# Kernel tuning notes

Hardware: AMD Instinct MI355X
Metric: run time of the kernel (lower is better)

Reference implementation:

```python
import jax, jax.numpy as jnp
import numpy as np
from jax import lax


def setup_inputs() -> dict:
    key = jax.random.key(0)
    # [C=512, H=256, W=256] feature map
    x = jax.random.normal(key, (512, 256, 256), dtype=jnp.float32)
    return {"x": x}


def reference(x):
    # Original torch forward mutates x in place: _bottom_pool (cummax down rows,
    # axis=1) modifies x and returns it, then _right_pool (cummax across cols,
    # axis=2) runs on the SAME already-bottom-pooled tensor. Thus `bottom` and
    # `right` alias and out = 2 * cummax_w(cummax_h(x)).
    y = lax.cummax(lax.cummax(x, axis=1), axis=2)
    return y + y
```

## Files before the change

kernel.cpp:

```cpp
#include <hip/hip_runtime.h>
#include <math.h>

#define CC 512
#define HH 256
#define WW 256
#define RB 32
#define NTILES (HH / RB)
#define NT 256
#define RPW (RB / 4)

typedef float f32x4 __attribute__((ext_vector_type(4)));

#define BAR()    asm volatile("s_barrier" ::: "memory")
#define WAITV(N) asm volatile("s_waitcnt vmcnt(" #N ")" ::: "memory")
#define WAITL()  asm volatile("s_waitcnt lgkmcnt(0)" ::: "memory")

template<int CTRL, int ROW_MASK>
__device__ __forceinline__ float dpp_ninf(float v) {
    union { float f; int i; } o, s, r;
    o.f = -INFINITY;
    s.f = v;
    r.i = __builtin_amdgcn_update_dpp(o.i, s.i, CTRL, ROW_MASK, 0xF, false);
    return r.f;
}

__device__ __forceinline__ float wave_incl_max(float v) {
    v = fmaxf(v, dpp_ninf<0x111, 0xF>(v));
    v = fmaxf(v, dpp_ninf<0x112, 0xF>(v));
    v = fmaxf(v, dpp_ninf<0x114, 0xF>(v));
    v = fmaxf(v, dpp_ninf<0x118, 0xF>(v));
    v = fmaxf(v, dpp_ninf<0x142, 0xA>(v));
    v = fmaxf(v, dpp_ninf<0x143, 0xC>(v));
    return v;
}

__device__ __forceinline__ void stage_rows(const float* src, float* lds_row_base,
                                           int wave, int lane) {
    #pragma unroll
    for (int i = 0; i < RPW; ++i) {
        int r = wave * RPW + i;
        const float* g = src + r * WW + lane * 4;
        __builtin_amdgcn_global_load_lds(
            (const __attribute__((address_space(1))) void*)g,
            (__attribute__((address_space(3))) void*)(lds_row_base + r * WW),
            16, 0, 0);
    }
}

__global__ __launch_bounds__(NT) void corner_pool_kernel(const float* __restrict__ x,
                                                         float* __restrict__ out) {
    __shared__ float tile[2][RB][WW];
    const int t    = threadIdx.x;
    const int lane = t & 63;
    const int wave = t >> 6;
    const int c    = blockIdx.x;

    const float* xc = x   + (size_t)c * HH * WW;
    float*       oc = out + (size_t)c * HH * WW;

    float cm = -INFINITY;

    stage_rows(xc, &tile[0][0][0], wave, lane);

    #pragma unroll
    for (int ti = 0; ti < NTILES; ++ti) {
        const int cb = ti & 1;

        if (ti + 1 < NTILES) {
            stage_rows(xc + (size_t)(ti + 1) * RB * WW, &tile[cb ^ 1][0][0], wave, lane);
            WAITV(8);
        } else {
            WAITV(0);
        }
        BAR();

        #pragma unroll
        for (int r = 0; r < RB; ++r) {
            cm = fmaxf(cm, tile[cb][r][t]);
            tile[cb][r][t] = cm;
        }
        WAITL();
        BAR();

        #pragma unroll
        for (int i = 0; i < RPW; ++i) {
            int r = wave * RPW + i;
            f32x4 v = *(const f32x4*)&tile[cb][r][lane * 4];
            float p0 = v.x;
            float p1 = fmaxf(p0, v.y);
            float p2 = fmaxf(p1, v.z);
            float p3 = fmaxf(p2, v.w);
            float s  = wave_incl_max(p3);
            float e  = dpp_ninf<0x138, 0xF>(s);
            f32x4 o;
            o.x = 2.0f * fmaxf(e, p0);
            o.y = 2.0f * fmaxf(e, p1);
            o.z = 2.0f * fmaxf(e, p2);
            o.w = 2.0f * fmaxf(e, p3);
            __builtin_nontemporal_store(o, (f32x4*)(oc + (size_t)(ti * RB + r) * WW + lane * 4));
        }
        BAR();
    }
}

extern "C" void kernel_launch(void* const* d_in, const int* in_sizes, int n_in,
                              void* d_out, int out_size, void* d_ws, size_t ws_size,
                              hipStream_t stream) {
    const float* x = (const float*)d_in[0];
    float* out = (float*)d_out;
    corner_pool_kernel<<<dim3(CC), dim3(NT), 0, stream>>>(x, out);
}
```

Baseline: 46.94 us.

## Replace LDS-staged sequential column scan with two-pass band-parallel scan

The kernel no longer scans each column sequentially through double-buffered LDS tiles. The channel is split into 8 row bands, one per wave. Each wave first reduces its band to per-column maxima, and these are combined in LDS to get a prefix carry. Each wave then re-reads its band to produce the scanned output directly from registers. This removes most LDS traffic and the barriers between tiles and exposes more parallelism, but it reads the input twice (about 7/8 extra reads, possibly served from L2/MALL).

```diff
diff --git a/kernel.cpp b/kernel.cpp
--- a/kernel.cpp
+++ b/kernel.cpp
@@ -4,16 +4,11 @@
 #define CC 512
 #define HH 256
 #define WW 256
-#define RB 32
-#define NTILES (HH / RB)
-#define NT 256
-#define RPW (RB / 4)
+#define NT 512
+#define NW (NT / 64)
+#define BH (HH / NW)
 
 typedef float f32x4 __attribute__((ext_vector_type(4)));
-
-#define BAR()    asm volatile("s_barrier" ::: "memory")
-#define WAITV(N) asm volatile("s_waitcnt vmcnt(" #N ")" ::: "memory")
-#define WAITL()  asm volatile("s_waitcnt lgkmcnt(0)" ::: "memory")
 
 template<int CTRL, int ROW_MASK>
 __device__ __forceinline__ float dpp_ninf(float v) {
@@ -34,72 +29,62 @@
     return v;
 }
 
-__device__ __forceinline__ void stage_rows(const float* src, float* lds_row_base,
-                                           int wave, int lane) {
-    #pragma unroll
-    for (int i = 0; i < RPW; ++i) {
-        int r = wave * RPW + i;
-        const float* g = src + r * WW + lane * 4;
-        __builtin_amdgcn_global_load_lds(
-            (const __attribute__((address_space(1))) void*)g,
-            (__attribute__((address_space(3))) void*)(lds_row_base + r * WW),
-            16, 0, 0);
-    }
+__device__ __forceinline__ f32x4 fmax4(f32x4 a, f32x4 b) {
+    f32x4 r;
+    r.x = fmaxf(a.x, b.x);
+    r.y = fmaxf(a.y, b.y);
+    r.z = fmaxf(a.z, b.z);
+    r.w = fmaxf(a.w, b.w);
+    return r;
 }
 
 __global__ __launch_bounds__(NT) void corner_pool_kernel(const float* __restrict__ x,
                                                          float* __restrict__ out) {
-    __shared__ float tile[2][RB][WW];
+    __shared__ f32x4 colmax[NW][64];
+
     const int t    = threadIdx.x;
     const int lane = t & 63;
-    const int wave = t >> 6;
+    const int w    = t >> 6;
     const int c    = blockIdx.x;
 
-    const float* xc = x   + (size_t)c * HH * WW;
-    float*       oc = out + (size_t)c * HH * WW;
+    const float* xc   = x   + (size_t)c * HH * WW;
+    float*       oc   = out + (size_t)c * HH * WW;
+    const float* band = xc + (size_t)w * BH * WW;
+    float*       ob   = oc + (size_t)w * BH * WW;
 
-    float cm = -INFINITY;
+    const f32x4 ninf4 = {-INFINITY, -INFINITY, -INFINITY, -INFINITY};
 
-    stage_rows(xc, &tile[0][0][0], wave, lane);
+    if (w < NW - 1) {
+        f32x4 m = ninf4;
+        #pragma unroll 8
+        for (int r = 0; r < BH; ++r) {
+            f32x4 v = *(const f32x4*)(band + r * WW + lane * 4);
+            m = fmax4(m, v);
+        }
+        colmax[w][lane] = m;
+    }
+    __syncthreads();
 
-    #pragma unroll
-    for (int ti = 0; ti < NTILES; ++ti) {
-        const int cb = ti & 1;
+    f32x4 cm = ninf4;
+    for (int b = 0; b < w; ++b)
+        cm = fmax4(cm, colmax[b][lane]);
 
-        if (ti + 1 < NTILES) {
-            stage_rows(xc + (size_t)(ti + 1) * RB * WW, &tile[cb ^ 1][0][0], wave, lane);
-            WAITV(8);
-        } else {
-            WAITV(0);
-        }
-        BAR();
-
-        #pragma unroll
-        for (int r = 0; r < RB; ++r) {
-            cm = fmaxf(cm, tile[cb][r][t]);
-            tile[cb][r][t] = cm;
-        }
-        WAITL();
-        BAR();
-
-        #pragma unroll
-        for (int i = 0; i < RPW; ++i) {
-            int r = wave * RPW + i;
-            f32x4 v = *(const f32x4*)&tile[cb][r][lane * 4];
-            float p0 = v.x;
-            float p1 = fmaxf(p0, v.y);
-            float p2 = fmaxf(p1, v.z);
-            float p3 = fmaxf(p2, v.w);
-            float s  = wave_incl_max(p3);
-            float e  = dpp_ninf<0x138, 0xF>(s);
-            f32x4 o;
-            o.x = 2.0f * fmaxf(e, p0);
-            o.y = 2.0f * fmaxf(e, p1);
-            o.z = 2.0f * fmaxf(e, p2);
-            o.w = 2.0f * fmaxf(e, p3);
-            __builtin_nontemporal_store(o, (f32x4*)(oc + (size_t)(ti * RB + r) * WW + lane * 4));
-        }
-        BAR();
+    #pragma unroll 8
+    for (int r = 0; r < BH; ++r) {
+        f32x4 v = *(const f32x4*)(band + r * WW + lane * 4);
+        cm = fmax4(cm, v);
+        float p0 = cm.x;
+        float p1 = fmaxf(p0, cm.y);
+        float p2 = fmaxf(p1, cm.z);
+        float p3 = fmaxf(p2, cm.w);
+        float s  = wave_incl_max(p3);
+        float e  = dpp_ninf<0x138, 0xF>(s);
+        f32x4 o;
+        o.x = 2.0f * fmaxf(e, p0);
+        o.y = 2.0f * fmaxf(e, p1);
+        o.z = 2.0f * fmaxf(e, p2);
+        o.w = 2.0f * fmaxf(e, p3);
+        __builtin_nontemporal_store(o, (f32x4*)(ob + (size_t)r * WW + lane * 4));
     }
 }
 
```

New measurement: 61.76 us. 31.6% more time.
